# Kernel tuning notes

Hardware: AMD Instinct MI355X
Metric: run time of the kernel (lower is better)

The kernel has to match this reference:

```python
import jax, jax.numpy as jnp
import numpy as np

EPS = 1e-5

def _layernorm(h):
    # parameter-free LayerNorm over last dim (elementwise_affine=False)
    mu = jnp.mean(h, axis=-1, keepdims=True)
    var = jnp.mean(jnp.square(h - mu), axis=-1, keepdims=True)
    return (h - mu) / jnp.sqrt(var + EPS)

def setup_inputs() -> dict:
    key = jax.random.key(0)
    k1, k2, k3, k4 = jax.random.split(key, 4)
    B, D, F_, I = 16, 37, 4096, 64
    x = jax.random.normal(k1, (B, D, F_), dtype=jnp.float32)
    s = 1.0 / np.sqrt(D)  # ~ torch Linear default init scale
    Wq = jax.random.normal(k2, (D, I), dtype=jnp.float32) * s
    Wk = jax.random.normal(k3, (D, I), dtype=jnp.float32) * s
    Wv = jax.random.normal(k4, (D, I), dtype=jnp.float32) * s
    return {"x": x, "Wq": Wq, "Wk": Wk, "Wv": Wv}

def reference(x, Wq, Wk, Wv):
    # x: [B, depth, featuresize] -> entities [B, F, depth]
    xb = jnp.transpose(x, (0, 2, 1))
    q = _layernorm(jnp.einsum('bfd,di->bfi', xb, Wq))
    k = _layernorm(jnp.einsum('bfd,di->bfi', xb, Wk))
    v = _layernorm(jnp.einsum('bfd,di->bfi', xb, Wv))
    d = q.shape[-1]
    att = jnp.einsum('bqi,bki->bqk', q, k) / jnp.sqrt(jnp.float32(d))
    # faithful to torch: softmax over dim=1 (the query axis), not the key axis
    weights = jax.nn.softmax(att, axis=-2)
    return jnp.einsum('bqk,bki->bqi', weights, v)
```

## Files before the change

kernel.cpp:

```cpp
#include <hip/hip_runtime.h>
#include <math.h>

#define B_  16
#define D_  37
#define F_  4096
#define I_  64
#define EPS 1e-5f
#define QSCALE 0.18033688011112042f
#define NQS 2

typedef unsigned short u16;
typedef __bf16 bf16x8 __attribute__((ext_vector_type(8)));
typedef __bf16 bf16x2v __attribute__((ext_vector_type(2)));
typedef float  f32x16 __attribute__((ext_vector_type(16)));
typedef float  f32x2v __attribute__((ext_vector_type(2)));
typedef unsigned int u32x4 __attribute__((ext_vector_type(4)));
typedef int i32x2 __attribute__((ext_vector_type(2)));

#define ZERO16 {0,0,0,0, 0,0,0,0, 0,0,0,0, 0,0,0,0}
#define MFMA32(a, b, c) __builtin_amdgcn_mfma_f32_32x32x16_bf16((a), (b), (c), 0, 0, 0)

#if __has_builtin(__builtin_amdgcn_exp2f)
#define EX2(x) __builtin_amdgcn_exp2f(x)
#else
#define EX2(x) exp2f(x)
#endif
#if __has_builtin(__builtin_amdgcn_rcpf)
#define RCP(x) __builtin_amdgcn_rcpf(x)
#else
#define RCP(x) (1.f / (x))
#endif

__device__ __forceinline__ u16 f2b(float f) {
  unsigned u = __builtin_bit_cast(unsigned, f);
  return (u16)((u + 0x7fffu + ((u >> 16) & 1u)) >> 16);
}
__device__ __forceinline__ float b2f(u16 h) {
  return __builtin_bit_cast(float, (unsigned)h << 16);
}
__device__ __forceinline__ unsigned pk2(float lo, float hi) {
  f32x2v f = {lo, hi};
  bf16x2v h = __builtin_convertvector(f, bf16x2v);
  return __builtin_bit_cast(unsigned, h);
}

__device__ __forceinline__ void plswap(unsigned& a, unsigned& b) {
#if __has_builtin(__builtin_amdgcn_permlane32_swap)
  i32x2 r = __builtin_amdgcn_permlane32_swap((int)a, (int)b, false, false);
  a = (unsigned)r[0];
  b = (unsigned)r[1];
#else
  const int lh = (int)((threadIdx.x & 63) >> 5);
  unsigned pa = (unsigned)__shfl_xor((int)a, 32, 64);
  unsigned pb = (unsigned)__shfl_xor((int)b, 32, 64);
  unsigned na = lh ? pb : a;
  unsigned nb = lh ? b : pa;
  a = na;
  b = nb;
#endif
}

__device__ __forceinline__ void build_af(const f32x16& s, bf16x8& f0, bf16x8& f1) {
  float e[16];
#pragma unroll
  for (int r = 0; r < 16; ++r) e[r] = EX2(s[r]);
  unsigned a = pk2(e[0], e[1]),   bq = pk2(e[2], e[3]);
  unsigned c = pk2(e[4], e[5]),   d  = pk2(e[6], e[7]);
  plswap(a, c);
  plswap(bq, d);
  u32x4 v0 = {a, bq, c, d};
  f0 = __builtin_bit_cast(bf16x8, v0);
  unsigned ee = pk2(e[8], e[9]),  ff = pk2(e[10], e[11]);
  unsigned g  = pk2(e[12], e[13]), h = pk2(e[14], e[15]);
  plswap(ee, g);
  plswap(ff, h);
  u32x4 v1 = {ee, ff, g, h};
  f1 = __builtin_bit_cast(bf16x8, v1);
}

__device__ __forceinline__ bf16x8 ldfrag(const u16* base, int row, int kb) {
  return *(const bf16x8*)(base + (row << 6) + ((kb ^ (row & 7)) << 3));
}
__device__ __forceinline__ void stage16(u16* dst, const u16* src, int c, int spitch) {
  const int r = c >> 3, cb = c & 7;
  const int4 v = *(const int4*)(src + (size_t)r * spitch + (cb << 3));
  *(int4*)(dst + (r << 6) + ((cb ^ (r & 7)) << 3)) = v;
}
__device__ __forceinline__ int soff_l(int c) {
  const int r = c >> 3, cb = c & 7;
  return (r << 6) + ((cb ^ (r & 7)) << 3);
}
__device__ __forceinline__ int soff_g(int c, int spitch) {
  return (c >> 3) * spitch + ((c & 7) << 3);
}

__global__ __launch_bounds__(256) void qkv_ln_k(
    const float* __restrict__ x,
    const float* __restrict__ Wq, const float* __restrict__ Wk,
    const float* __restrict__ Wv,
    u16* __restrict__ qn, u16* __restrict__ kn, u16* __restrict__ vt) {
  __shared__ float sW[3 * D_ * I_];
  __shared__ float xs[D_ * 64];
  __shared__ __align__(16) u16 vtile[64 * 72];

  const int t = threadIdx.x;
  const int b = blockIdx.y;
  const int f0 = blockIdx.x * 64;

  for (int i = t; i < D_ * I_; i += 256) {
    sW[i]               = Wq[i];
    sW[D_ * I_ + i]     = Wk[i];
    sW[2 * D_ * I_ + i] = Wv[i];
  }
  const float* xb = x + (size_t)b * D_ * F_ + f0;
  for (int i = t; i < D_ * 64; i += 256)
    xs[i] = xb[(size_t)(i >> 6) * F_ + (i & 63)];
  __syncthreads();

  const int lane = t & 63, w = t >> 6;

  for (int it = 0; it < 16; ++it) {
    const int fl = w * 16 + it;
    float hq = 0.f, hk = 0.f, hv = 0.f;
#pragma unroll
    for (int d = 0; d < D_; ++d) {
      const float xv = xs[d * 64 + fl];
      hq = fmaf(xv, sW[d * 64 + lane], hq);
      hk = fmaf(xv, sW[D_ * I_ + d * 64 + lane], hk);
      hv = fmaf(xv, sW[2 * D_ * I_ + d * 64 + lane], hv);
    }
    auto lnorm = [&](float a) -> float {
      float s = a;
#pragma unroll
      for (int o = 32; o > 0; o >>= 1) s += __shfl_xor(s, o, 64);
      const float mu = s * (1.f / 64.f);
      const float d0 = a - mu;
      float v = d0 * d0;
#pragma unroll
      for (int o = 32; o > 0; o >>= 1) v += __shfl_xor(v, o, 64);
      return d0 * rsqrtf(v * (1.f / 64.f) + EPS);
    };
    const size_t fo = ((size_t)b * F_ + f0 + fl) * I_ + lane;
    qn[fo] = f2b(lnorm(hq) * QSCALE);
    kn[fo] = f2b(lnorm(hk));
    vtile[lane * 72 + fl] = f2b(lnorm(hv));
  }
  __syncthreads();
  for (int p = 0; p < 2; ++p) {
    const int c = p * 256 + t;
    const int r = c >> 3, off = (c & 7) * 8;
    const int4 v = *(const int4*)&vtile[r * 72 + off];
    *(int4*)(vt + ((size_t)b * I_ + r) * F_ + f0 + off) = v;
  }
}

__global__ __launch_bounds__(256, 2) void attn_stats_k(
    const u16* __restrict__ qn, const u16* __restrict__ kn,
    float* __restrict__ zp) {
  __shared__ __align__(16) u16 sm[16384];

  const int t = threadIdx.x, lane = t & 63, w = t >> 6;
  const int l31 = lane & 31, lh = lane >> 5;
  const int b = blockIdx.y, k0 = blockIdx.x * 256, qh = blockIdx.z;

  const u16* kb = kn + ((size_t)b * F_ + k0) * I_;
#pragma unroll
  for (int p = 0; p < 8; ++p) stage16(sm, kb, p * 256 + t, 64);
  __syncthreads();
  bf16x8 kf[2][4];
#pragma unroll
  for (int kb2 = 0; kb2 < 2; ++kb2)
#pragma unroll
    for (int ic = 0; ic < 4; ++ic)
      kf[kb2][ic] = ldfrag(sm + (w * 64 + kb2 * 32) * 64, l31, ic * 2 + lh);
  __syncthreads();

  int qoff_l[2], qoff_g[2];
#pragma unroll
  for (int p = 0; p < 2; ++p) {
    const int c = p * 256 + t;
    qoff_l[p] = soff_l(c);
    qoff_g[p] = soff_g(c, 64);
  }

  const u16* qsrc = qn + ((size_t)b * F_ + qh * (F_ / NQS)) * I_;
#pragma unroll
  for (int p = 0; p < 2; ++p)
    *(int4*)(sm + qoff_l[p]) = *(const int4*)(qsrc + qoff_g[p]);
  qsrc += 64 * I_;

  float Zc[2][2] = {{0.f, 0.f}, {0.f, 0.f}};
  const int NC = F_ / NQS / 64;

  for (int c = 0; c < NC; ++c) {
    const int cur = (c & 1) * 4096;
    __syncthreads();
    if (c + 1 < NC) {
      const int nxt = cur ^ 4096;
#pragma unroll
      for (int p = 0; p < 2; ++p)
        *(int4*)(sm + nxt + qoff_l[p]) = *(const int4*)(qsrc + qoff_g[p]);
      qsrc += 64 * I_;
    }

    f32x16 a00 = ZERO16, a01 = ZERO16, a10 = ZERO16, a11 = ZERO16;
#pragma unroll
    for (int ic = 0; ic < 4; ++ic) {
      const bf16x8 q0f = ldfrag(sm + cur, l31, ic * 2 + lh);
      const bf16x8 q1f = ldfrag(sm + cur + 32 * 64, l31, ic * 2 + lh);
      a00 = MFMA32(q0f, kf[0][ic], a00);
      a01 = MFMA32(q0f, kf[1][ic], a01);
      a10 = MFMA32(q1f, kf[0][ic], a10);
      a11 = MFMA32(q1f, kf[1][ic], a11);
    }
#pragma unroll
    for (int r = 0; r < 16; ++r) {
      Zc[0][0] += EX2(a00[r]);
      Zc[0][1] += EX2(a01[r]);
      Zc[1][0] += EX2(a10[r]);
      Zc[1][1] += EX2(a11[r]);
    }
  }

#pragma unroll
  for (int kb2 = 0; kb2 < 2; ++kb2) {
    float Zt = Zc[0][kb2] + Zc[1][kb2];
    Zt += __shfl_xor(Zt, 32, 64);
    if (lane < 32)
      zp[((size_t)qh * B_ + b) * F_ + k0 + w * 64 + kb2 * 32 + lane] = Zt;
  }
}

__global__ __launch_bounds__(256) void vscale_k(u16* __restrict__ vt,
                                                const float* __restrict__ zp) {
  const int b = blockIdx.y;
  const int off = (blockIdx.x * 256 + (int)threadIdx.x) * 8;
  const int k = off & (F_ - 1);
  u16* p = vt + (size_t)b * I_ * F_ + off;
  const float* z0 = zp + (size_t)b * F_ + k;
  const float* z1 = zp + (size_t)B_ * F_ + (size_t)b * F_ + k;
  int4 raw = *(const int4*)p;
  u16 es[8], os[8];
  *(int4*)es = raw;
#pragma unroll
  for (int j = 0; j < 8; ++j) {
    const float v = b2f(es[j]);
    const float rz = RCP(z0[j] + z1[j]);
    os[j] = f2b(v * rz);
  }
  *(int4*)p = *(int4*)os;
}

__global__ __launch_bounds__(128, 2) void attn_out_k(
    const u16* __restrict__ qn, const u16* __restrict__ kn,
    const u16* __restrict__ vt, float* __restrict__ out,
    u16* __restrict__ pout) {
  __shared__ __align__(16) u16 sm[16384];

  const int t = threadIdx.x, lane = t & 63, w = t >> 6;
  const int l31 = lane & 31, lh = lane >> 5;
  const int b = blockIdx.y, q0 = blockIdx.x * 128, ks = blockIdx.z;

  const u16* qb = qn + ((size_t)b * F_ + q0) * I_;
#pragma unroll
  for (int p = 0; p < 8; ++p) stage16(sm, qb, p * 128 + t, 64);
  __syncthreads();
  bf16x8 qf[2][4];
#pragma unroll
  for (int qb2 = 0; qb2 < 2; ++qb2)
#pragma unroll
    for (int ic = 0; ic < 4; ++ic)
      qf[qb2][ic] = ldfrag(sm + (w * 64 + qb2 * 32) * 64, l31, ic * 2 + lh);
  __syncthreads();

  int off_l[4], kg[4], vg[4];
#pragma unroll
  for (int p = 0; p < 4; ++p) {
    const int c = p * 128 + t;
    off_l[p] = soff_l(c);
    kg[p] = soff_g(c, 64);
    vg[p] = soff_g(c, F_);
  }

  const u16* ksrc = kn + ((size_t)b * F_ + ks * (F_ / 2)) * I_;
  const u16* vsrc = vt + (size_t)b * I_ * F_ + ks * (F_ / 2);
#pragma unroll
  for (int p = 0; p < 4; ++p) {
    *(int4*)(sm + off_l[p])        = *(const int4*)(ksrc + kg[p]);
    *(int4*)(sm + 8192 + off_l[p]) = *(const int4*)(vsrc + vg[p]);
  }
  ksrc += 64 * I_;
  vsrc += 64;

  f32x16 o00 = ZERO16, o01 = ZERO16, o10 = ZERO16, o11 = ZERO16;
  const int NC = F_ / 2 / 64;

  for (int c = 0; c < NC; ++c) {
    const int cur = (c & 1) * 4096;
    __syncthreads();
    if (c + 1 < NC) {
      const int nxt = cur ^ 4096;
#pragma unroll
      for (int p = 0; p < 4; ++p) {
        *(int4*)(sm + nxt + off_l[p])        = *(const int4*)(ksrc + kg[p]);
        *(int4*)(sm + 8192 + nxt + off_l[p]) = *(const int4*)(vsrc + vg[p]);
      }
      ksrc += 64 * I_;
      vsrc += 64;
    }

    const u16* Kc = sm + cur;
    f32x16 s00 = ZERO16, s01 = ZERO16, s10 = ZERO16, s11 = ZERO16;
#pragma unroll
    for (int ic = 0; ic < 4; ++ic) {
      const bf16x8 ak0 = ldfrag(Kc, l31, ic * 2 + lh);
      const bf16x8 ak1 = ldfrag(Kc + 32 * 64, l31, ic * 2 + lh);
      s00 = MFMA32(ak0, qf[0][ic], s00);
      s01 = MFMA32(ak0, qf[1][ic], s01);
      s10 = MFMA32(ak1, qf[0][ic], s10);
      s11 = MFMA32(ak1, qf[1][ic], s11);
    }

    bf16x8 af[2][4];
    build_af(s00, af[0][0], af[0][1]);
    build_af(s10, af[0][2], af[0][3]);
    build_af(s01, af[1][0], af[1][1]);
    build_af(s11, af[1][2], af[1][3]);

    const u16* Vc = sm + 8192 + cur;
#pragma unroll
    for (int kb4 = 0; kb4 < 4; ++kb4) {
      const bf16x8 bv0 = ldfrag(Vc, l31, kb4 * 2 + lh);
      const bf16x8 bv1 = ldfrag(Vc + 32 * 64, l31, kb4 * 2 + lh);
      o00 = MFMA32(af[0][kb4], bv0, o00);
      o01 = MFMA32(af[0][kb4], bv1, o01);
      o10 = MFMA32(af[1][kb4], bv0, o10);
      o11 = MFMA32(af[1][kb4], bv1, o11);
    }
  }

  if (ks == 0) {
    float* ob = out + ((size_t)b * F_ + q0 + w * 64) * I_;
#pragma unroll
    for (int r = 0; r < 16; ++r) {
      const int qr = (r & 3) + 8 * (r >> 2) + 4 * lh;
      ob[(size_t)qr * I_ + l31]              = o00[r];
      ob[(size_t)qr * I_ + 32 + l31]         = o01[r];
      ob[(size_t)(32 + qr) * I_ + l31]       = o10[r];
      ob[(size_t)(32 + qr) * I_ + 32 + l31]  = o11[r];
    }
  } else {
    u16* pb = pout + ((size_t)b * F_ + q0 + w * 64) * I_;
#pragma unroll
    for (int r = 0; r < 16; ++r) {
      const int qr = (r & 3) + 8 * (r >> 2) + 4 * lh;
      pb[(size_t)qr * I_ + l31]              = f2b(o00[r]);
      pb[(size_t)qr * I_ + 32 + l31]         = f2b(o01[r]);
      pb[(size_t)(32 + qr) * I_ + l31]       = f2b(o10[r]);
      pb[(size_t)(32 + qr) * I_ + 32 + l31]  = f2b(o11[r]);
    }
  }
}

__global__ __launch_bounds__(256) void reduce_k(float* __restrict__ out,
                                                const u16* __restrict__ pout) {
  const size_t i = ((size_t)blockIdx.x * 256 + threadIdx.x) * 8;
  float4 a0 = *(const float4*)(out + i);
  float4 a1 = *(const float4*)(out + i + 4);
  int4 praw = *(const int4*)(pout + i);
  u16 es[8];
  *(int4*)es = praw;
  a0.x += b2f(es[0]); a0.y += b2f(es[1]); a0.z += b2f(es[2]); a0.w += b2f(es[3]);
  a1.x += b2f(es[4]); a1.y += b2f(es[5]); a1.z += b2f(es[6]); a1.w += b2f(es[7]);
  *(float4*)(out + i)     = a0;
  *(float4*)(out + i + 4) = a1;
}

extern "C" void kernel_launch(void* const* d_in, const int* in_sizes, int n_in,
                              void* d_out, int out_size, void* d_ws,
                              size_t ws_size, hipStream_t stream) {
  const float* x  = (const float*)d_in[0];
  const float* Wq = (const float*)d_in[1];
  const float* Wk = (const float*)d_in[2];
  const float* Wv = (const float*)d_in[3];
  float* out = (float*)d_out;

  const size_t NBF = (size_t)B_ * F_ * I_;
  u16* qn   = (u16*)d_ws;
  u16* kn   = qn + NBF;
  u16* vt   = kn + NBF;
  float* zp = (float*)(vt + NBF);
  u16* pout = (u16*)(zp + (size_t)NQS * B_ * F_);

  qkv_ln_k<<<dim3(F_ / 64, B_), 256, 0, stream>>>(x, Wq, Wk, Wv, qn, kn, vt);
  attn_stats_k<<<dim3(F_ / 256, B_, NQS), 256, 0, stream>>>(qn, kn, zp);
  vscale_k<<<dim3(I_ * F_ / 2048, B_), 256, 0, stream>>>(vt, zp);
  attn_out_k<<<dim3(F_ / 128, B_, 2), 128, 0, stream>>>(qn, kn, vt, out, pout);
  reduce_k<<<dim3((int)(NBF / 2048)), 256, 0, stream>>>(out, pout);
}
```

Baseline: 241.9 us.

## Register-staged prefetch, finer wave split in attention kernels, more stats splits

Global loads for the next Q/K/V chunk now go into registers before the barrier and are stored to shared memory after the MFMA work, overlapping memory latency with compute. attn_out_k switches to 256-thread blocks with each wave owning 32 queries, trading fewer accumulators per wave for more waves. attn_stats_k splits queries into four parts instead of two, and vscale sums the extra partials. MFMA sections are wrapped in s_setprio. Smaller per-wave tiles raise LDS fragment reloads per MFMA.

```diff
diff --git a/kernel.cpp b/kernel.cpp
--- a/kernel.cpp
+++ b/kernel.cpp
@@ -7,7 +7,7 @@
 #define I_  64
 #define EPS 1e-5f
 #define QSCALE 0.18033688011112042f
-#define NQS 2
+#define NQS 4
 
 typedef unsigned short u16;
 typedef __bf16 bf16x8 __attribute__((ext_vector_type(8)));
@@ -154,7 +154,7 @@
   }
 }
 
-__global__ __launch_bounds__(256, 2) void attn_stats_k(
+__global__ __launch_bounds__(256, 4) void attn_stats_k(
     const u16* __restrict__ qn, const u16* __restrict__ kn,
     float* __restrict__ zp) {
   __shared__ __align__(16) u16 sm[16384];
@@ -194,16 +194,17 @@
 
   for (int c = 0; c < NC; ++c) {
     const int cur = (c & 1) * 4096;
+    int4 qr0, qr1;
+    const bool pf = (c + 1 < NC);
+    if (pf) {
+      qr0 = *(const int4*)(qsrc + qoff_g[0]);
+      qr1 = *(const int4*)(qsrc + qoff_g[1]);
+      qsrc += 64 * I_;
+    }
     __syncthreads();
-    if (c + 1 < NC) {
-      const int nxt = cur ^ 4096;
-#pragma unroll
-      for (int p = 0; p < 2; ++p)
-        *(int4*)(sm + nxt + qoff_l[p]) = *(const int4*)(qsrc + qoff_g[p]);
-      qsrc += 64 * I_;
-    }
 
     f32x16 a00 = ZERO16, a01 = ZERO16, a10 = ZERO16, a11 = ZERO16;
+    __builtin_amdgcn_s_setprio(1);
 #pragma unroll
     for (int ic = 0; ic < 4; ++ic) {
       const bf16x8 q0f = ldfrag(sm + cur, l31, ic * 2 + lh);
@@ -213,6 +214,7 @@
       a10 = MFMA32(q1f, kf[0][ic], a10);
       a11 = MFMA32(q1f, kf[1][ic], a11);
     }
+    __builtin_amdgcn_s_setprio(0);
 #pragma unroll
     for (int r = 0; r < 16; ++r) {
       Zc[0][0] += EX2(a00[r]);
@@ -220,6 +222,12 @@
       Zc[1][0] += EX2(a10[r]);
       Zc[1][1] += EX2(a11[r]);
     }
+
+    if (pf) {
+      const int nxt = cur ^ 4096;
+      *(int4*)(sm + nxt + qoff_l[0]) = qr0;
+      *(int4*)(sm + nxt + qoff_l[1]) = qr1;
+    }
   }
 
 #pragma unroll
@@ -236,22 +244,24 @@
   const int b = blockIdx.y;
   const int off = (blockIdx.x * 256 + (int)threadIdx.x) * 8;
   const int k = off & (F_ - 1);
+  const size_t BF = (size_t)B_ * F_;
   u16* p = vt + (size_t)b * I_ * F_ + off;
-  const float* z0 = zp + (size_t)b * F_ + k;
-  const float* z1 = zp + (size_t)B_ * F_ + (size_t)b * F_ + k;
+  const float* z = zp + (size_t)b * F_ + k;
   int4 raw = *(const int4*)p;
   u16 es[8], os[8];
   *(int4*)es = raw;
 #pragma unroll
   for (int j = 0; j < 8; ++j) {
     const float v = b2f(es[j]);
-    const float rz = RCP(z0[j] + z1[j]);
-    os[j] = f2b(v * rz);
+    float zs = 0.f;
+#pragma unroll
+    for (int qh = 0; qh < NQS; ++qh) zs += z[qh * BF + j];
+    os[j] = f2b(v * RCP(zs));
   }
   *(int4*)p = *(int4*)os;
 }
 
-__global__ __launch_bounds__(128, 2) void attn_out_k(
+__global__ __launch_bounds__(256, 4) void attn_out_k(
     const u16* __restrict__ qn, const u16* __restrict__ kn,
     const u16* __restrict__ vt, float* __restrict__ out,
     u16* __restrict__ pout) {
@@ -263,20 +273,18 @@
 
   const u16* qb = qn + ((size_t)b * F_ + q0) * I_;
 #pragma unroll
-  for (int p = 0; p < 8; ++p) stage16(sm, qb, p * 128 + t, 64);
-  __syncthreads();
-  bf16x8 qf[2][4];
-#pragma unroll
-  for (int qb2 = 0; qb2 < 2; ++qb2)
-#pragma unroll
-    for (int ic = 0; ic < 4; ++ic)
-      qf[qb2][ic] = ldfrag(sm + (w * 64 + qb2 * 32) * 64, l31, ic * 2 + lh);
-  __syncthreads();
-
-  int off_l[4], kg[4], vg[4];
-#pragma unroll
-  for (int p = 0; p < 4; ++p) {
-    const int c = p * 128 + t;
+  for (int p = 0; p < 4; ++p) stage16(sm, qb, p * 256 + t, 64);
+  __syncthreads();
+  bf16x8 qf[4];
+#pragma unroll
+  for (int ic = 0; ic < 4; ++ic)
+    qf[ic] = ldfrag(sm + (w * 32) * 64, l31, ic * 2 + lh);
+  __syncthreads();
+
+  int off_l[2], kg[2], vg[2];
+#pragma unroll
+  for (int p = 0; p < 2; ++p) {
+    const int c = p * 256 + t;
     off_l[p] = soff_l(c);
     kg[p] = soff_g(c, 64);
     vg[p] = soff_g(c, F_);
@@ -285,79 +293,81 @@
   const u16* ksrc = kn + ((size_t)b * F_ + ks * (F_ / 2)) * I_;
   const u16* vsrc = vt + (size_t)b * I_ * F_ + ks * (F_ / 2);
 #pragma unroll
-  for (int p = 0; p < 4; ++p) {
+  for (int p = 0; p < 2; ++p) {
     *(int4*)(sm + off_l[p])        = *(const int4*)(ksrc + kg[p]);
     *(int4*)(sm + 8192 + off_l[p]) = *(const int4*)(vsrc + vg[p]);
   }
   ksrc += 64 * I_;
   vsrc += 64;
 
-  f32x16 o00 = ZERO16, o01 = ZERO16, o10 = ZERO16, o11 = ZERO16;
+  f32x16 o0 = ZERO16, o1 = ZERO16;
   const int NC = F_ / 2 / 64;
 
   for (int c = 0; c < NC; ++c) {
     const int cur = (c & 1) * 4096;
-    __syncthreads();
-    if (c + 1 < NC) {
-      const int nxt = cur ^ 4096;
-#pragma unroll
-      for (int p = 0; p < 4; ++p) {
-        *(int4*)(sm + nxt + off_l[p])        = *(const int4*)(ksrc + kg[p]);
-        *(int4*)(sm + 8192 + nxt + off_l[p]) = *(const int4*)(vsrc + vg[p]);
-      }
+    int4 kr0, kr1, vr0, vr1;
+    const bool pf = (c + 1 < NC);
+    if (pf) {
+      kr0 = *(const int4*)(ksrc + kg[0]);
+      kr1 = *(const int4*)(ksrc + kg[1]);
+      vr0 = *(const int4*)(vsrc + vg[0]);
+      vr1 = *(const int4*)(vsrc + vg[1]);
       ksrc += 64 * I_;
       vsrc += 64;
     }
+    __syncthreads();
 
     const u16* Kc = sm + cur;
-    f32x16 s00 = ZERO16, s01 = ZERO16, s10 = ZERO16, s11 = ZERO16;
+    f32x16 s0 = ZERO16, s1 = ZERO16;
+    __builtin_amdgcn_s_setprio(1);
 #pragma unroll
     for (int ic = 0; ic < 4; ++ic) {
       const bf16x8 ak0 = ldfrag(Kc, l31, ic * 2 + lh);
       const bf16x8 ak1 = ldfrag(Kc + 32 * 64, l31, ic * 2 + lh);
-      s00 = MFMA32(ak0, qf[0][ic], s00);
-      s01 = MFMA32(ak0, qf[1][ic], s01);
-      s10 = MFMA32(ak1, qf[0][ic], s10);
-      s11 = MFMA32(ak1, qf[1][ic], s11);
-    }
-
-    bf16x8 af[2][4];
-    build_af(s00, af[0][0], af[0][1]);
-    build_af(s10, af[0][2], af[0][3]);
-    build_af(s01, af[1][0], af[1][1]);
-    build_af(s11, af[1][2], af[1][3]);
+      s0 = MFMA32(ak0, qf[ic], s0);
+      s1 = MFMA32(ak1, qf[ic], s1);
+    }
+    __builtin_amdgcn_s_setprio(0);
+
+    bf16x8 af[4];
+    build_af(s0, af[0], af[1]);
+    build_af(s1, af[2], af[3]);
 
     const u16* Vc = sm + 8192 + cur;
+    __builtin_amdgcn_s_setprio(1);
 #pragma unroll
     for (int kb4 = 0; kb4 < 4; ++kb4) {
       const bf16x8 bv0 = ldfrag(Vc, l31, kb4 * 2 + lh);
       const bf16x8 bv1 = ldfrag(Vc + 32 * 64, l31, kb4 * 2 + lh);
-      o00 = MFMA32(af[0][kb4], bv0, o00);
-      o01 = MFMA32(af[0][kb4], bv1, o01);
-      o10 = MFMA32(af[1][kb4], bv0, o10);
-      o11 = MFMA32(af[1][kb4], bv1, o11);
+      o0 = MFMA32(af[kb4], bv0, o0);
+      o1 = MFMA32(af[kb4], bv1, o1);
+    }
+    __builtin_amdgcn_s_setprio(0);
+
+    if (pf) {
+      const int nxt = cur ^ 4096;
+      *(int4*)(sm + nxt + off_l[0])        = kr0;
+      *(int4*)(sm + nxt + off_l[1])        = kr1;
+      *(int4*)(sm + 8192 + nxt + off_l[0]) = vr0;
+      *(int4*)(sm + 8192 + nxt + off_l[1]) = vr1;
     }
   }
 
   if (ks == 0) {
-    float* ob = out + ((size_t)b * F_ + q0 + w * 64) * I_;
+    float* ob = out + ((size_t)b * F_ + q0 + w * 32) * I_;
 #pragma unroll
     for (int r = 0; r < 16; ++r) {
       const int qr = (r & 3) + 8 * (r >> 2) + 4 * lh;
-      ob[(size_t)qr * I_ + l31]              = o00[r];
-      ob[(size_t)qr * I_ + 32 + l31]         = o01[r];
-      ob[(size_t)(32 + qr) * I_ + l31]       = o10[r];
-      ob[(size_t)(32 + qr) * I_ + 32 + l31]  = o11[r];
+      ob[(size_t)qr * I_ + l31]      = o0[r];
+      ob[(size_t)qr * I_ + 32 + l31] = o1[r];
     }
   } else {
-    u16* pb = pout + ((size_t)b * F_ + q0 + w * 64) * I_;
+    u16* pb = pout + ((size_t)b * F_ + q0 + w * 32) * I_;
 #pragma unroll
     for (int r = 0; r < 16; ++r) {
       const int qr = (r & 3) + 8 * (r >> 2) + 4 * lh;
-      pb[(size_t)qr * I_ + l31]              = f2b(o00[r]);
-      pb[(size_t)qr * I_ + 32 + l31]         = f2b(o01[r]);
-      pb[(size_t)(32 + qr) * I_ + l31]       = f2b(o10[r]);
-      pb[(size_t)(32 + qr) * I_ + 32 + l31]  = f2b(o11[r]);
+      pb[(size_t)qr * I_ + l31]      = f2b(o0[r]);
+      pb[(size_t)qr * I_ + 32 + l31] = f2b(o1[r]);
     }
   }
 }
@@ -395,6 +405,6 @@
   qkv_ln_k<<<dim3(F_ / 64, B_), 256, 0, stream>>>(x, Wq, Wk, Wv, qn, kn, vt);
   attn_stats_k<<<dim3(F_ / 256, B_, NQS), 256, 0, stream>>>(qn, kn, zp);
   vscale_k<<<dim3(I_ * F_ / 2048, B_), 256, 0, stream>>>(vt, zp);
-  attn_out_k<<<dim3(F_ / 128, B_, 2), 128, 0, stream>>>(qn, kn, vt, out, pout);
+  attn_out_k<<<dim3(F_ / 128, B_, 2), 256, 0, stream>>>(qn, kn, vt, out, pout);
   reduce_k<<<dim3((int)(NBF / 2048)), 256, 0, stream>>>(out, pout);
 }
```

Result: no change. 244.0 us (+0.9%).
